# Kernel tuning notes

Measured on AMD Instinct MI355X. Metric: run time of the kernel, lower is better.

Reference implementation:

```python
import jax, jax.numpy as jnp
import numpy as np

HEADS = 8
DIM_HEAD = 64
SCALE = DIM_HEAD ** -0.5


def setup_inputs() -> dict:
    key = jax.random.key(0)
    ks = jax.random.split(key, 5)
    B, N, D = 2, 4096, 512
    x = jax.random.normal(ks[0], (B, N, D), dtype=jnp.float32)
    Wq = jax.random.normal(ks[1], (D, D), dtype=jnp.float32) * (D ** -0.5)
    Wk = jax.random.normal(ks[2], (D, D), dtype=jnp.float32) * (D ** -0.5)
    Wv = jax.random.normal(ks[3], (D, D), dtype=jnp.float32) * (D ** -0.5)
    Wo = jax.random.normal(ks[4], (D, D), dtype=jnp.float32) * (D ** -0.5)
    bo = jnp.zeros((D,), dtype=jnp.float32)
    return {"x": x, "Wq": Wq, "Wk": Wk, "Wv": Wv, "Wo": Wo, "bo": bo}


def reference(x, Wq, Wk, Wv, Wo, bo):
    B, N, D = x.shape
    h, d = HEADS, DIM_HEAD
    # torch nn.Linear: y = x @ W.T
    q = (x @ Wq.T).reshape(B, N, h, d).transpose(0, 2, 1, 3)  # b h n d
    k = (x @ Wk.T).reshape(B, N, h, d).transpose(0, 2, 1, 3)
    v = (x @ Wv.T).reshape(B, N, h, d).transpose(0, 2, 1, 3)
    # fp32 score path (ATTN_PRECISION='fp32')
    sim = jnp.einsum('bhid,bhjd->bhij', q.astype(jnp.float32), k.astype(jnp.float32)) * SCALE
    attn = jax.nn.softmax(sim, axis=-1).astype(v.dtype)
    out = jnp.einsum('bhij,bhjd->bhid', attn, v)  # b h n d
    out = out.transpose(0, 2, 1, 3).reshape(B, N, h * d)  # b n (h d)
    return out @ Wo.T + bo
```

## Files before the change

### kernel.cpp

```cpp
#include <hip/hip_runtime.h>
#include <hip/hip_bf16.h>

#define B_ 2
#define N_ 4096
#define D_ 512
#define H_ 8
#define M_ (B_*N_)
#define QSCALE_ 0.18033688011f

typedef short bf16x8 __attribute__((ext_vector_type(8)));
typedef float f32x4  __attribute__((ext_vector_type(4)));

static __device__ __forceinline__ unsigned short f2bf(float f) {
    union { float f; unsigned int u; } v; v.f = f;
    unsigned int r = v.u + 0x7fffu + ((v.u >> 16) & 1u);
    return (unsigned short)(r >> 16);
}
static __device__ __forceinline__ float bf2f(unsigned short h) {
    union { unsigned int u; float f; } v; v.u = ((unsigned int)h) << 16;
    return v.f;
}
static __device__ __forceinline__ unsigned int cvt_pk_bf16(float a, float b) {
    unsigned int r;
    asm("v_cvt_pk_bf16_f32 %0, %1, %2" : "=v"(r) : "v"(a), "v"(b));
    return r;
}
static __device__ __forceinline__ float lo_bf(unsigned int w) { return __uint_as_float(w << 16); }
static __device__ __forceinline__ float hi_bf(unsigned int w) { return __uint_as_float(w & 0xffff0000u); }

__global__ void conv_split(const float* __restrict__ src, unsigned short* __restrict__ dh,
                           unsigned short* __restrict__ dl, int n4)
{
    int i = blockIdx.x * blockDim.x + threadIdx.x;
    const int stride = gridDim.x * blockDim.x;
    for (; i < n4; i += stride) {
        float4 v = ((const float4*)src)[i];
        ushort4 hv, lv;
        hv.x = f2bf(v.x); hv.y = f2bf(v.y); hv.z = f2bf(v.z); hv.w = f2bf(v.w);
        lv.x = f2bf(v.x - bf2f(hv.x)); lv.y = f2bf(v.y - bf2f(hv.y));
        lv.z = f2bf(v.z - bf2f(hv.z)); lv.w = f2bf(v.w - bf2f(hv.w));
        ((ushort4*)dh)[i] = hv;
        ((ushort4*)dl)[i] = lv;
    }
}

__global__ void conv_w4(const float* __restrict__ w0, const float* __restrict__ w1,
                        const float* __restrict__ w2, const float* __restrict__ w3,
                        unsigned short* __restrict__ dh, unsigned short* __restrict__ dl)
{
    const int which = blockIdx.y;
    const float* src = which == 0 ? w0 : which == 1 ? w1 : which == 2 ? w2 : w3;
    const int i = blockIdx.x * 256 + threadIdx.x;
    float4 v = ((const float4*)src)[i];
    ushort4 hv, lv;
    hv.x = f2bf(v.x); hv.y = f2bf(v.y); hv.z = f2bf(v.z); hv.w = f2bf(v.w);
    lv.x = f2bf(v.x - bf2f(hv.x)); lv.y = f2bf(v.y - bf2f(hv.y));
    lv.z = f2bf(v.z - bf2f(hv.z)); lv.w = f2bf(v.w - bf2f(hv.w));
    ((ushort4*)(dh + (size_t)which * 262144))[i] = hv;
    ((ushort4*)(dl + (size_t)which * 262144))[i] = lv;
}

template<int MODE>
__global__ __launch_bounds__(256, 2) void gemm_mfma(
    const unsigned short* __restrict__ Ah, const unsigned short* __restrict__ Al,
    const unsigned short* __restrict__ Wh, const unsigned short* __restrict__ Wl,
    const float* __restrict__ bias, float* __restrict__ outF,
    unsigned short* __restrict__ oh0, unsigned short* __restrict__ ol0,
    unsigned short* __restrict__ oh1, unsigned short* __restrict__ ol1,
    float scale0)
{
    __shared__ unsigned short At[2][8192];
    __shared__ unsigned short Bt[2][8192];

    const int t = threadIdx.x;
    const int lane = t & 63, wave = t >> 6;
    const int l15 = lane & 15, g = lane >> 4;
    const int wr = wave >> 1, wc = wave & 1;
    const int mb = blockIdx.x * 128;

    int which = 0, nbeff;
    if (MODE == 1) { which = blockIdx.y >> 2; nbeff = (blockIdx.y & 3) * 128; }
    else           { nbeff = blockIdx.y * 128; }
    const unsigned short* Whp = Wh + (size_t)which * 262144;
    const unsigned short* Wlp = Wl + (size_t)which * 262144;

    const int srow = t >> 1, sh = t & 1;
    const size_t gAr = (size_t)(mb + srow) * 512 + sh * 16;
    const size_t gBr = (size_t)(nbeff + srow) * 512 + sh * 16;
    const int sw = srow & 7;
    const int dA0 = srow * 64 + (((sh * 2 + 0) ^ sw) * 8);
    const int dA1 = srow * 64 + (((sh * 2 + 1) ^ sw) * 8);
    const int dA2 = srow * 64 + (((sh * 2 + 4) ^ sw) * 8);
    const int dA3 = srow * 64 + (((sh * 2 + 5) ^ sw) * 8);

    bf16x8 sA[4], sB[4];
#define GLOAD(K0) do {                                                              \
        sA[0] = *(const bf16x8*)&Ah[gAr + (K0)];  sA[1] = *(const bf16x8*)&Ah[gAr + (K0) + 8];  \
        sA[2] = *(const bf16x8*)&Al[gAr + (K0)];  sA[3] = *(const bf16x8*)&Al[gAr + (K0) + 8];  \
        sB[0] = *(const bf16x8*)&Whp[gBr + (K0)]; sB[1] = *(const bf16x8*)&Whp[gBr + (K0) + 8]; \
        sB[2] = *(const bf16x8*)&Wlp[gBr + (K0)]; sB[3] = *(const bf16x8*)&Wlp[gBr + (K0) + 8]; \
    } while (0)
#define SWRITE(BB) do {                                                             \
        *(bf16x8*)&At[BB][dA0] = sA[0]; *(bf16x8*)&At[BB][dA1] = sA[1];             \
        *(bf16x8*)&At[BB][dA2] = sA[2]; *(bf16x8*)&At[BB][dA3] = sA[3];             \
        *(bf16x8*)&Bt[BB][dA0] = sB[0]; *(bf16x8*)&Bt[BB][dA1] = sB[1];             \
        *(bf16x8*)&Bt[BB][dA2] = sB[2]; *(bf16x8*)&Bt[BB][dA3] = sB[3];             \
    } while (0)

    f32x4 acc[4][4];
#pragma unroll
    for (int mi = 0; mi < 4; ++mi)
#pragma unroll
        for (int ni = 0; ni < 4; ++ni) acc[mi][ni] = (f32x4){0.f, 0.f, 0.f, 0.f};

    GLOAD(0); SWRITE(0); __syncthreads();
    int cur = 0;
    for (int ks = 0; ks < 16; ++ks) {
        if (ks < 15) GLOAD((ks + 1) * 32);

        bf16x8 afh[4], afl[4], wfh[4], wfl[4];
#pragma unroll
        for (int mi = 0; mi < 4; ++mi) {
            const int ar = wr * 64 + mi * 16 + l15, asw = ar & 7;
            afh[mi] = *(const bf16x8*)&At[cur][ar * 64 + ((g ^ asw) * 8)];
            afl[mi] = *(const bf16x8*)&At[cur][ar * 64 + (((g + 4) ^ asw) * 8)];
        }
#pragma unroll
        for (int ni = 0; ni < 4; ++ni) {
            const int br = wc * 64 + ni * 16 + l15, bsw = br & 7;
            wfh[ni] = *(const bf16x8*)&Bt[cur][br * 64 + ((g ^ bsw) * 8)];
            wfl[ni] = *(const bf16x8*)&Bt[cur][br * 64 + (((g + 4) ^ bsw) * 8)];
        }
#pragma unroll
        for (int mi = 0; mi < 4; ++mi)
#pragma unroll
            for (int ni = 0; ni < 4; ++ni) {
                acc[mi][ni] = __builtin_amdgcn_mfma_f32_16x16x32_bf16(afh[mi], wfh[ni], acc[mi][ni], 0, 0, 0);
                acc[mi][ni] = __builtin_amdgcn_mfma_f32_16x16x32_bf16(afl[mi], wfh[ni], acc[mi][ni], 0, 0, 0);
                acc[mi][ni] = __builtin_amdgcn_mfma_f32_16x16x32_bf16(afh[mi], wfl[ni], acc[mi][ni], 0, 0, 0);
            }

        if (ks < 15) SWRITE(cur ^ 1);
        __syncthreads();
        cur ^= 1;
    }
#undef GLOAD
#undef SWRITE

    if (MODE == 0) {
#pragma unroll
        for (int ni = 0; ni < 4; ++ni) {
            const int col = nbeff + wc * 64 + ni * 16 + l15;
            const float bv = bias[col];
#pragma unroll
            for (int mi = 0; mi < 4; ++mi) {
                const int m0 = mb + wr * 64 + mi * 16 + g * 4;
#pragma unroll
                for (int r = 0; r < 4; ++r)
                    outF[(size_t)(m0 + r) * 512 + col] = acc[mi][ni][r] + bv;
            }
        }
    } else if (MODE == 1) {
        unsigned short* oh = which ? oh1 : oh0;
        unsigned short* ol = which ? ol1 : ol0;
        const float scl = which ? 1.0f : scale0;
#pragma unroll
        for (int ni = 0; ni < 4; ++ni) {
            const int col = nbeff + wc * 64 + ni * 16 + l15;
            const int hh = col >> 6, dd = col & 63;
#pragma unroll
            for (int mi = 0; mi < 4; ++mi) {
                const int m0 = mb + wr * 64 + mi * 16 + g * 4;
                const int b = m0 >> 12, seq0 = m0 & (N_ - 1);
                const size_t base = ((size_t)(b * H_ + hh) * N_ + seq0) * 64 + dd;
#pragma unroll
                for (int r = 0; r < 4; ++r) {
                    const float s = acc[mi][ni][r] * scl;
                    const unsigned short hv = f2bf(s);
                    oh[base + (size_t)r * 64] = hv;
                    ol[base + (size_t)r * 64] = f2bf(s - bf2f(hv));
                }
            }
        }
    } else {
#pragma unroll
        for (int ni = 0; ni < 4; ++ni) {
            const int col = nbeff + wc * 64 + ni * 16 + l15;
            const int hh = col >> 6, dd = col & 63;
#pragma unroll
            for (int mi = 0; mi < 4; ++mi) {
                const int m0 = mb + wr * 64 + mi * 16 + g * 4;
                const int b = m0 >> 12, seq0 = m0 & (N_ - 1);
                const size_t base = ((size_t)((b * H_ + hh) * 64) + dd) * N_ + seq0;
                const float s0 = acc[mi][ni][0], s1 = acc[mi][ni][1],
                            s2 = acc[mi][ni][2], s3 = acc[mi][ni][3];
                ushort4 hv, lv;
                hv.x = f2bf(s0); hv.y = f2bf(s1); hv.z = f2bf(s2); hv.w = f2bf(s3);
                lv.x = f2bf(s0 - bf2f(hv.x)); lv.y = f2bf(s1 - bf2f(hv.y));
                lv.z = f2bf(s2 - bf2f(hv.z)); lv.w = f2bf(s3 - bf2f(hv.w));
                *(ushort4*)&oh0[base] = hv;
                *(ushort4*)&ol0[base] = lv;
            }
        }
    }
}

__global__ __launch_bounds__(256, 2) void attn_mfma(
    const unsigned short* __restrict__ qh, const unsigned short* __restrict__ ql,
    const unsigned short* __restrict__ kh, const unsigned short* __restrict__ kl,
    const unsigned short* __restrict__ vth, const unsigned short* __restrict__ vtl,
    unsigned short* __restrict__ oh, unsigned short* __restrict__ ol)
{
    __shared__ unsigned short Kb[2][2][4096];
    __shared__ unsigned short Vb[2][2][4096];

    const int t    = threadIdx.x;
    const int lane = t & 63;
    const int wave = t >> 6;
    const int l15  = lane & 15;
    const int g    = lane >> 4;
    const int bh   = blockIdx.y;
    const int qbase = blockIdx.x * 128 + wave * 32;

    bf16x8 qf[2][2][2];
#pragma unroll
    for (int rt = 0; rt < 2; ++rt)
#pragma unroll
        for (int c = 0; c < 2; ++c) {
            const size_t src = ((size_t)bh * N_ + qbase + rt * 16 + l15) * 64 + c * 32 + g * 8;
            qf[rt][c][0] = *(const bf16x8*)&qh[src];
            qf[rt][c][1] = *(const bf16x8*)&ql[src];
        }

    f32x4 O[2][4];
#pragma unroll
    for (int rt = 0; rt < 2; ++rt)
#pragma unroll
        for (int dt = 0; dt < 4; ++dt) O[rt][dt] = (f32x4){0.f, 0.f, 0.f, 0.f};
    float mreg[2] = {-3.0e38f, -3.0e38f};
    float lreg[2] = {0.f, 0.f};

    const int srow = t >> 3;
    const int sc16 = t & 7;
    const size_t kbase = (size_t)bh * N_ * 64;
    const size_t vbase = (size_t)bh * 64 * N_;
    const int vdst0 = srow * 64 + ((sc16 ^ (srow & 7)) * 8);
    const int vdst1 = (srow + 32) * 64 + ((sc16 ^ ((srow + 32) & 7)) * 8);
    const int krho  = (((srow >> 2) & 1) << 4) | (((srow >> 3) & 3) << 2) | (srow & 3);
    const int kdst0 = krho * 64 + ((sc16 ^ (krho & 7)) * 8);
    const int kdst1 = kdst0 + 32 * 64;

    bf16x8 sKh[2], sKl[2], sVh[2], sVl[2];

#define LOADT(KT) do {                                                          \
        const size_t gK0 = kbase + ((size_t)((KT) * 64 + srow)) * 64 + sc16 * 8;      \
        const size_t gK1 = kbase + ((size_t)((KT) * 64 + srow + 32)) * 64 + sc16 * 8; \
        const size_t gV0 = vbase + (size_t)srow * N_ + (KT) * 64 + sc16 * 8;          \
        const size_t gV1 = vbase + (size_t)(srow + 32) * N_ + (KT) * 64 + sc16 * 8;   \
        sKh[0] = *(const bf16x8*)&kh[gK0];  sKh[1] = *(const bf16x8*)&kh[gK1];  \
        sKl[0] = *(const bf16x8*)&kl[gK0];  sKl[1] = *(const bf16x8*)&kl[gK1];  \
        sVh[0] = *(const bf16x8*)&vth[gV0]; sVh[1] = *(const bf16x8*)&vth[gV1]; \
        sVl[0] = *(const bf16x8*)&vtl[gV0]; sVl[1] = *(const bf16x8*)&vtl[gV1]; \
    } while (0)

#define WRITET(BB) do {                                                         \
        *(bf16x8*)&Kb[BB][0][kdst0] = sKh[0]; *(bf16x8*)&Kb[BB][0][kdst1] = sKh[1]; \
        *(bf16x8*)&Kb[BB][1][kdst0] = sKl[0]; *(bf16x8*)&Kb[BB][1][kdst1] = sKl[1]; \
        *(bf16x8*)&Vb[BB][0][vdst0] = sVh[0]; *(bf16x8*)&Vb[BB][0][vdst1] = sVh[1]; \
        *(bf16x8*)&Vb[BB][1][vdst0] = sVl[0]; *(bf16x8*)&Vb[BB][1][vdst1] = sVl[1]; \
    } while (0)

    LOADT(0);
    WRITET(0);
    __syncthreads();

    int cur = 0;
    for (int kt = 0; kt < N_ / 64; ++kt) {
        const bool pf = (kt + 1 < N_ / 64);
        if (pf) LOADT(kt + 1);

        f32x4 S[2][4];
#pragma unroll
        for (int rt = 0; rt < 2; ++rt)
#pragma unroll
            for (int j = 0; j < 4; ++j) S[rt][j] = (f32x4){0.f, 0.f, 0.f, 0.f};

#pragma unroll
        for (int j = 0; j < 4; ++j) {
            const int krow = j * 16 + l15;
            const int rb = krow * 64, sw2 = (krow & 7) * 8;
#pragma unroll
            for (int c = 0; c < 2; ++c) {
                const int off = rb + (((c * 4 + g) * 8) ^ sw2);
                bf16x8 kfh = *(const bf16x8*)&Kb[cur][0][off];
                bf16x8 kfl = *(const bf16x8*)&Kb[cur][1][off];
#pragma unroll
                for (int rt = 0; rt < 2; ++rt) {
                    S[rt][j] = __builtin_amdgcn_mfma_f32_16x16x32_bf16(kfh, qf[rt][c][0], S[rt][j], 0, 0, 0);
                    S[rt][j] = __builtin_amdgcn_mfma_f32_16x16x32_bf16(kfl, qf[rt][c][0], S[rt][j], 0, 0, 0);
                    S[rt][j] = __builtin_amdgcn_mfma_f32_16x16x32_bf16(kfh, qf[rt][c][1], S[rt][j], 0, 0, 0);
                }
            }
        }

        bf16x8 pah[2][2], pal[2][2];
#pragma unroll
        for (int rt = 0; rt < 2; ++rt) {
            float pmax = -3.0e38f;
#pragma unroll
            for (int j = 0; j < 4; ++j)
#pragma unroll
                for (int r = 0; r < 4; ++r) pmax = fmaxf(pmax, S[rt][j][r]);
            pmax = fmaxf(pmax, __shfl_xor(pmax, 16));
            pmax = fmaxf(pmax, __shfl_xor(pmax, 32));

            const float mold = mreg[rt];
            if (!__all(pmax <= mold + 8.0f)) {
                const float mnew = fmaxf(mold, pmax);
                const float alpha = exp2f(mold - mnew);
#pragma unroll
                for (int dt = 0; dt < 4; ++dt)
#pragma unroll
                    for (int r = 0; r < 4; ++r) O[rt][dt][r] *= alpha;
                lreg[rt] *= alpha;
                mreg[rt] = mnew;
            }
            const float mb2 = mreg[rt];

            float lsum = 0.f;
#pragma unroll
            for (int j = 0; j < 4; ++j)
#pragma unroll
                for (int r = 0; r < 4; ++r) {
                    S[rt][j][r] = exp2f(S[rt][j][r] - mb2);
                    lsum += S[rt][j][r];
                }
            lreg[rt] += lsum;

#pragma unroll
            for (int c = 0; c < 2; ++c) {
                const f32x4 s0 = S[rt][2 * c], s1 = S[rt][2 * c + 1];
                union { unsigned int u[4]; bf16x8 v; } th, tl;
                th.u[0] = cvt_pk_bf16(s0[0], s0[1]);
                th.u[1] = cvt_pk_bf16(s0[2], s0[3]);
                th.u[2] = cvt_pk_bf16(s1[0], s1[1]);
                th.u[3] = cvt_pk_bf16(s1[2], s1[3]);
                tl.u[0] = cvt_pk_bf16(s0[0] - lo_bf(th.u[0]), s0[1] - hi_bf(th.u[0]));
                tl.u[1] = cvt_pk_bf16(s0[2] - lo_bf(th.u[1]), s0[3] - hi_bf(th.u[1]));
                tl.u[2] = cvt_pk_bf16(s1[0] - lo_bf(th.u[2]), s1[1] - hi_bf(th.u[2]));
                tl.u[3] = cvt_pk_bf16(s1[2] - lo_bf(th.u[3]), s1[3] - hi_bf(th.u[3]));
                pah[rt][c] = th.v;
                pal[rt][c] = tl.v;
            }
        }

#pragma unroll
        for (int c = 0; c < 2; ++c) {
#pragma unroll
            for (int dt = 0; dt < 4; ++dt) {
                const int vrow = dt * 16 + l15;
                const int off = vrow * 64 + (((c * 4 + g) * 8) ^ ((vrow & 7) * 8));
                bf16x8 vfh = *(const bf16x8*)&Vb[cur][0][off];
                bf16x8 vfl = *(const bf16x8*)&Vb[cur][1][off];
#pragma unroll
                for (int rt = 0; rt < 2; ++rt) {
                    O[rt][dt] = __builtin_amdgcn_mfma_f32_16x16x32_bf16(vfh, pah[rt][c], O[rt][dt], 0, 0, 0);
                    O[rt][dt] = __builtin_amdgcn_mfma_f32_16x16x32_bf16(vfl, pah[rt][c], O[rt][dt], 0, 0, 0);
                    O[rt][dt] = __builtin_amdgcn_mfma_f32_16x16x32_bf16(vfh, pal[rt][c], O[rt][dt], 0, 0, 0);
                }
            }
        }

        if (pf) WRITET(cur ^ 1);
        __syncthreads();
        cur ^= 1;
    }

    const int b = bh >> 3, hh = bh & 7;
#pragma unroll
    for (int rt = 0; rt < 2; ++rt) {
        float lt = lreg[rt];
        lt += __shfl_xor(lt, 16);
        lt += __shfl_xor(lt, 32);
        const float inv = 1.0f / lt;
        const int n = qbase + rt * 16 + l15;
        const size_t rowbase = ((size_t)(b * N_) + n) * 512 + hh * 64 + g * 4;
#pragma unroll
        for (int dt = 0; dt < 4; ++dt) {
            const float s0 = O[rt][dt][0] * inv, s1 = O[rt][dt][1] * inv,
                        s2 = O[rt][dt][2] * inv, s3 = O[rt][dt][3] * inv;
            ushort4 hv, lv;
            hv.x = f2bf(s0); hv.y = f2bf(s1); hv.z = f2bf(s2); hv.w = f2bf(s3);
            lv.x = f2bf(s0 - bf2f(hv.x)); lv.y = f2bf(s1 - bf2f(hv.y));
            lv.z = f2bf(s2 - bf2f(hv.z)); lv.w = f2bf(s3 - bf2f(hv.w));
            *(ushort4*)&oh[rowbase + dt * 16] = hv;
            *(ushort4*)&ol[rowbase + dt * 16] = lv;
        }
    }
#undef LOADT
#undef WRITET
}

extern "C" void kernel_launch(void* const* d_in, const int* in_sizes, int n_in,
                              void* d_out, int out_size, void* d_ws, size_t ws_size,
                              hipStream_t stream)
{
    const float* x  = (const float*)d_in[0];
    const float* Wq = (const float*)d_in[1];
    const float* Wk = (const float*)d_in[2];
    const float* Wv = (const float*)d_in[3];
    const float* Wo = (const float*)d_in[4];
    const float* bo = (const float*)d_in[5];

    unsigned char* w8 = (unsigned char*)d_ws;
    const size_t MB = 1024 * 1024;
    unsigned short* xh  = (unsigned short*)(w8);
    unsigned short* xl  = (unsigned short*)(w8 + 8  * MB);
    unsigned short* wh  = (unsigned short*)(w8 + 16 * MB);
    unsigned short* wl  = (unsigned short*)(w8 + 18 * MB);
    unsigned short* qh  = (unsigned short*)(w8 + 20 * MB);
    unsigned short* ql  = (unsigned short*)(w8 + 28 * MB);
    unsigned short* kh  = (unsigned short*)(w8 + 36 * MB);
    unsigned short* kl  = (unsigned short*)(w8 + 44 * MB);
    unsigned short* vth = (unsigned short*)(w8 + 52 * MB);
    unsigned short* vtl = (unsigned short*)(w8 + 60 * MB);
    unsigned short* ah = xh;
    unsigned short* al = xl;
    float* out = (float*)d_out;

    conv_split<<<1024, 256, 0, stream>>>(x, xh, xl, M_ * 512 / 4);
    conv_w4<<<dim3(256, 4), 256, 0, stream>>>(Wq, Wk, Wv, Wo, wh, wl);

    gemm_mfma<1><<<dim3(64, 8), 256, 0, stream>>>(xh, xl, wh, wl, nullptr, nullptr,
                                                  qh, ql, kh, kl, QSCALE_);
    gemm_mfma<2><<<dim3(64, 4), 256, 0, stream>>>(xh, xl, wh + 2 * 262144, wl + 2 * 262144,
                                                  nullptr, nullptr, vth, vtl, nullptr, nullptr, 1.0f);

    attn_mfma<<<dim3(N_ / 128, 16), 256, 0, stream>>>(qh, ql, kh, kl, vth, vtl, ah, al);

    gemm_mfma<0><<<dim3(64, 4), 256, 0, stream>>>(ah, al, wh + 3 * 262144, wl + 3 * 262144,
                                                  bo, out, nullptr, nullptr, nullptr, nullptr, 1.0f);
}
```

Measured before the change: 365.7 us.

## Fuse QKV projections into one launch, drop P low-part MFMA, add setprio

Merges the Q/K and V projection GEMMs into a single launch with a 64x12 grid, where blocks with which==2 write the transposed V layout. The attention kernel stops splitting the softmax probabilities into hi/lo bf16 parts, removing one of the three MFMAs per PV tile. It also raises wave priority around the MFMA-heavy QK and PV loops. The aim is to cut launch overhead, conversion ALU work and matrix-core work, at the cost of lower precision in the PV product (P is now kept only as single bf16).

```diff
diff --git a/kernel.cpp b/kernel.cpp
--- a/kernel.cpp
+++ b/kernel.cpp
@@ -25,8 +25,6 @@
     asm("v_cvt_pk_bf16_f32 %0, %1, %2" : "=v"(r) : "v"(a), "v"(b));
     return r;
 }
-static __device__ __forceinline__ float lo_bf(unsigned int w) { return __uint_as_float(w << 16); }
-static __device__ __forceinline__ float hi_bf(unsigned int w) { return __uint_as_float(w & 0xffff0000u); }
 
 __global__ void conv_split(const float* __restrict__ src, unsigned short* __restrict__ dh,
                            unsigned short* __restrict__ dl, int n4)
@@ -67,6 +65,7 @@
     const float* __restrict__ bias, float* __restrict__ outF,
     unsigned short* __restrict__ oh0, unsigned short* __restrict__ ol0,
     unsigned short* __restrict__ oh1, unsigned short* __restrict__ ol1,
+    unsigned short* __restrict__ oh2, unsigned short* __restrict__ ol2,
     float scale0)
 {
     __shared__ unsigned short At[2][8192];
@@ -160,7 +159,7 @@
                     outF[(size_t)(m0 + r) * 512 + col] = acc[mi][ni][r] + bv;
             }
         }
-    } else if (MODE == 1) {
+    } else if (which < 2) {
         unsigned short* oh = which ? oh1 : oh0;
         unsigned short* ol = which ? ol1 : ol0;
         const float scl = which ? 1.0f : scale0;
@@ -198,8 +197,8 @@
                 hv.x = f2bf(s0); hv.y = f2bf(s1); hv.z = f2bf(s2); hv.w = f2bf(s3);
                 lv.x = f2bf(s0 - bf2f(hv.x)); lv.y = f2bf(s1 - bf2f(hv.y));
                 lv.z = f2bf(s2 - bf2f(hv.z)); lv.w = f2bf(s3 - bf2f(hv.w));
-                *(ushort4*)&oh0[base] = hv;
-                *(ushort4*)&ol0[base] = lv;
+                *(ushort4*)&oh2[base] = hv;
+                *(ushort4*)&ol2[base] = lv;
             }
         }
     }
@@ -285,6 +284,7 @@
 #pragma unroll
             for (int j = 0; j < 4; ++j) S[rt][j] = (f32x4){0.f, 0.f, 0.f, 0.f};
 
+        __builtin_amdgcn_s_setprio(1);
 #pragma unroll
         for (int j = 0; j < 4; ++j) {
             const int krow = j * 16 + l15;
@@ -302,8 +302,9 @@
                 }
             }
         }
-
-        bf16x8 pah[2][2], pal[2][2];
+        __builtin_amdgcn_s_setprio(0);
+
+        bf16x8 pah[2][2];
 #pragma unroll
         for (int rt = 0; rt < 2; ++rt) {
             float pmax = -3.0e38f;
@@ -340,20 +341,16 @@
 #pragma unroll
             for (int c = 0; c < 2; ++c) {
                 const f32x4 s0 = S[rt][2 * c], s1 = S[rt][2 * c + 1];
-                union { unsigned int u[4]; bf16x8 v; } th, tl;
+                union { unsigned int u[4]; bf16x8 v; } th;
                 th.u[0] = cvt_pk_bf16(s0[0], s0[1]);
                 th.u[1] = cvt_pk_bf16(s0[2], s0[3]);
                 th.u[2] = cvt_pk_bf16(s1[0], s1[1]);
                 th.u[3] = cvt_pk_bf16(s1[2], s1[3]);
-                tl.u[0] = cvt_pk_bf16(s0[0] - lo_bf(th.u[0]), s0[1] - hi_bf(th.u[0]));
-                tl.u[1] = cvt_pk_bf16(s0[2] - lo_bf(th.u[1]), s0[3] - hi_bf(th.u[1]));
-                tl.u[2] = cvt_pk_bf16(s1[0] - lo_bf(th.u[2]), s1[1] - hi_bf(th.u[2]));
-                tl.u[3] = cvt_pk_bf16(s1[2] - lo_bf(th.u[3]), s1[3] - hi_bf(th.u[3]));
                 pah[rt][c] = th.v;
-                pal[rt][c] = tl.v;
-            }
-        }
-
+            }
+        }
+
+        __builtin_amdgcn_s_setprio(1);
 #pragma unroll
         for (int c = 0; c < 2; ++c) {
 #pragma unroll
@@ -366,10 +363,10 @@
                 for (int rt = 0; rt < 2; ++rt) {
                     O[rt][dt] = __builtin_amdgcn_mfma_f32_16x16x32_bf16(vfh, pah[rt][c], O[rt][dt], 0, 0, 0);
                     O[rt][dt] = __builtin_amdgcn_mfma_f32_16x16x32_bf16(vfl, pah[rt][c], O[rt][dt], 0, 0, 0);
-                    O[rt][dt] = __builtin_amdgcn_mfma_f32_16x16x32_bf16(vfh, pal[rt][c], O[rt][dt], 0, 0, 0);
                 }
             }
         }
+        __builtin_amdgcn_s_setprio(0);
 
         if (pf) WRITET(cur ^ 1);
         __syncthreads();
@@ -431,13 +428,12 @@
     conv_split<<<1024, 256, 0, stream>>>(x, xh, xl, M_ * 512 / 4);
     conv_w4<<<dim3(256, 4), 256, 0, stream>>>(Wq, Wk, Wv, Wo, wh, wl);
 
-    gemm_mfma<1><<<dim3(64, 8), 256, 0, stream>>>(xh, xl, wh, wl, nullptr, nullptr,
-                                                  qh, ql, kh, kl, QSCALE_);
-    gemm_mfma<2><<<dim3(64, 4), 256, 0, stream>>>(xh, xl, wh + 2 * 262144, wl + 2 * 262144,
-                                                  nullptr, nullptr, vth, vtl, nullptr, nullptr, 1.0f);
+    gemm_mfma<1><<<dim3(64, 12), 256, 0, stream>>>(xh, xl, wh, wl, nullptr, nullptr,
+                                                   qh, ql, kh, kl, vth, vtl, QSCALE_);
 
     attn_mfma<<<dim3(N_ / 128, 16), 256, 0, stream>>>(qh, ql, kh, kl, vth, vtl, ah, al);
 
     gemm_mfma<0><<<dim3(64, 4), 256, 0, stream>>>(ah, al, wh + 3 * 262144, wl + 3 * 262144,
-                                                  bo, out, nullptr, nullptr, nullptr, nullptr, 1.0f);
-}
+                                                  bo, out, nullptr, nullptr, nullptr, nullptr,
+                                                  nullptr, nullptr, 1.0f);
+}
```

Result: faster. 323.5 us (-11.5%).
